# Kernel tuning notes

Measured on AMD Instinct MI355X. Metric: run time of the kernel, lower is better.

## Reference

```python
import jax, jax.numpy as jnp
import numpy as np

B, S, E, NUM_CLASSES = 4, 4096, 256, 16

def setup_inputs() -> dict:
    key = jax.random.key(0)
    ks = jax.random.split(key, 10)
    std = E ** -0.5
    return {
        "x":  jax.random.normal(ks[0], (B, S, E), dtype=jnp.float32),
        "wq": jax.random.normal(ks[1], (E, E), dtype=jnp.float32) * std,
        "bq": jnp.zeros((E,), dtype=jnp.float32),
        "wk": jax.random.normal(ks[2], (E, E), dtype=jnp.float32) * std,
        "bk": jnp.zeros((E,), dtype=jnp.float32),
        "wv": jax.random.normal(ks[3], (E, E), dtype=jnp.float32) * std,
        "bv": jnp.zeros((E,), dtype=jnp.float32),
        "wo": jax.random.normal(ks[4], (NUM_CLASSES, E), dtype=jnp.float32) * std,
        "bo": jnp.zeros((NUM_CLASSES,), dtype=jnp.float32),
    }

def reference(x, wq, bq, wk, bk, wv, bv, wo, bo):
    embed_dim = wq.shape[0]
    scaling = embed_dim ** -0.5  # float(embed_dim) ** (-0.5)
    # torch Linear: y = x @ W.T + b
    Q = jnp.einsum('bse,oe->bso', x, wq) + bq
    K = jnp.einsum('bse,oe->bso', x, wk) + bk
    V = jnp.einsum('bse,oe->bso', x, wv) + bv
    # scores: [B, S, S]
    scores = jnp.einsum('bqe,bke->bqk', Q, K) * scaling
    # original code has `/ (embed_dim ^ 0.5)`; intended math is / sqrt(embed_dim)
    attn = jax.nn.softmax(scores, axis=-1) * scaling
    attn_out = jnp.einsum('bqk,bke->bqe', attn, V)
    return jnp.einsum('bqe,oe->bqo', attn_out, wo) + bo
```

## Files before the change

### kernel.cpp

```cpp
#include <hip/hip_runtime.h>
#include <hip/hip_bf16.h>


#define S_ 4096
#define E_ 256
#define B_ 4
#define NC_ 16
#define BS_ (B_ * S_)
#define NS_ 4

typedef __attribute__((ext_vector_type(8))) short bf16x8;
typedef __attribute__((ext_vector_type(4))) float f32x4;

__device__ __forceinline__ unsigned short bf16_rtne(float f) {
    unsigned int u = __float_as_uint(f);
    return (unsigned short)((u + 0x7FFFu + ((u >> 16) & 1u)) >> 16);
}
__device__ __forceinline__ bf16x8 pack8(f32x4 a, f32x4 b) {
    bf16x8 r;
#pragma unroll
    for (int i = 0; i < 4; i++) r[i] = (short)bf16_rtne(a[i]);
#pragma unroll
    for (int i = 0; i < 4; i++) r[4 + i] = (short)bf16_rtne(b[i]);
    return r;
}
__device__ __forceinline__ void gl_lds16(const void* g, void* lds) {
    __builtin_amdgcn_global_load_lds(
        (const __attribute__((address_space(1))) unsigned int*)g,
        (__attribute__((address_space(3))) unsigned int*)lds, 16, 0, 0);
}
__device__ __forceinline__ int swz_u(int q) { return q ^ ((q >> 3) & 7); }

#define XUNITS_ (BS_ * E_ / 8)
#define WUNITS_ (3 * E_ * E_ / 8)
__global__ __launch_bounds__(256) void pack_xw(
    const float* __restrict__ x, const float* __restrict__ wq,
    const float* __restrict__ wk, const float* __restrict__ wv,
    short* __restrict__ xb, short* __restrict__ wb) {
    int u = blockIdx.x * 256 + threadIdx.x;
    const float* src;
    short* dst;
    if (u < XUNITS_) {
        src = x + (size_t)u * 8;
        dst = xb + (size_t)u * 8;
    } else {
        int u2 = u - XUNITS_;
        int sel = u2 >> 13;
        int off = (u2 & 8191) * 8;
        src = ((sel == 0) ? wq : (sel == 1) ? wk : wv) + off;
        dst = wb + sel * (E_ * E_) + off;
    }
    f32x4 a = *(const f32x4*)src;
    f32x4 b = *(const f32x4*)(src + 4);
    *(bf16x8*)dst = pack8(a, b);
}

__global__ __launch_bounds__(256) void qkv_gemm(
    const short* __restrict__ xb, const short* __restrict__ wb,
    const float* __restrict__ bq, const float* __restrict__ bk,
    const float* __restrict__ bv, short* __restrict__ Qb,
    short* __restrict__ Kb, short* __restrict__ Vtc) {
    __shared__ __align__(16) short stg[2][10240];
    __shared__ __align__(16) short epi[16896];

    int t = threadIdx.x;
    int lin = blockIdx.x;
    int xcd = lin & 7, r8 = lin >> 3;
    int sel = r8 >> 5;
    int m0 = (((xcd << 5) | (r8 & 31))) * 64;
    int lane = t & 63, wid = t >> 6, quad = lane >> 4, idx = lane & 15;

    const short* wsel = wb + sel * (E_ * E_);
    const float* bias = (sel == 0) ? bq : (sel == 1) ? bk : bv;

    int ux = swz_u(t);
    const short* xsrc = xb + (size_t)(m0 + (ux >> 2)) * E_ + (ux & 3) * 8;
    const short* wsrc[4];
#pragma unroll
    for (int i = 0; i < 4; i++) {
        int q = i * 256 + t, u = swz_u(q);
        wsrc[i] = wsel + (size_t)(u >> 2) * E_ + (u & 3) * 8;
    }

    gl_lds16(xsrc, &stg[0][t * 8]);
#pragma unroll
    for (int i = 0; i < 4; i++) gl_lds16(wsrc[i], &stg[0][(256 + i * 256 + t) * 8]);

    f32x4 zf = {0.f, 0.f, 0.f, 0.f};
    f32x4 acc[16];
#pragma unroll
    for (int i = 0; i < 16; i++) acc[i] = zf;

    int fo = (idx * 4 + quad) ^ (idx >> 1);

    for (int it = 0; it < 8; it++) {
        __syncthreads();
        if (it < 7) {
            int kc = (it + 1) * 32;
            short* d = stg[(it + 1) & 1];
            gl_lds16(xsrc + kc, &d[t * 8]);
#pragma unroll
            for (int i = 0; i < 4; i++)
                gl_lds16(wsrc[i] + kc, &d[(256 + i * 256 + t) * 8]);
        }
        const short* cb = stg[it & 1];
        bf16x8 af = *(const bf16x8*)&cb[(wid * 64 + fo) * 8];
        const short* cw = &cb[(256 + fo) * 8];
        __builtin_amdgcn_s_setprio(1);
#pragma unroll
        for (int ct = 0; ct < 16; ct++)
            acc[ct] = __builtin_amdgcn_mfma_f32_16x16x32_bf16(
                af, *(const bf16x8*)&cw[ct * 512], acc[ct], 0, 0, 0);
        __builtin_amdgcn_s_setprio(0);
    }

    int qr = quad * 4;
    if (sel == 2) {
#pragma unroll
        for (int ct = 0; ct < 16; ct++) {
            int e = ct * 16 + idx;
            float bb = bias[e];
#pragma unroll
            for (int r = 0; r < 4; r++) {
                int mr = wid * 16 + qr + r;
                int ckg = mr >> 5, sin = mr & 31;
                int sp = ((sin & 15) << 1) | (sin >> 4);
                int pos = (sp >> 3) ^ ((e >> 1) & 3);
                epi[ckg * 8192 + e * 32 + pos * 8 + (sp & 7)] =
                    (short)bf16_rtne(acc[ct][r] + bb);
            }
        }
        __syncthreads();
        size_t base = ((size_t)((m0 >> 12) * 128 + ((m0 & (S_ - 1)) >> 5))) * 8192;
#pragma unroll
        for (int j = 0; j < 8; j++) {
            int unit = j * 256 + t;
            *(bf16x8*)(Vtc + base + (size_t)unit * 8) = *(const bf16x8*)&epi[unit * 8];
        }
    } else {
        float alpha = (sel == 0) ? 0.0625f : 1.0f;
#pragma unroll
        for (int ct = 0; ct < 16; ct++) {
            int n = ct * 16 + idx;
            float bb = bias[n];
#pragma unroll
            for (int r = 0; r < 4; r++) {
                int row = wid * 16 + qr + r;
                int col = (sel == 1) ? ((((n >> 3) ^ (row & 7)) << 3) | (n & 7)) : n;
                epi[row * 264 + col] = (short)bf16_rtne((acc[ct][r] + bb) * alpha);
            }
        }
        __syncthreads();
        short* out = (sel == 0) ? Qb : Kb;
#pragma unroll
        for (int j = 0; j < 8; j++) {
            int g = j * 256 + t;
            int row = g >> 5, seg = g & 31;
            *(bf16x8*)(out + (size_t)(m0 + row) * E_ + seg * 8) =
                *(const bf16x8*)&epi[row * 264 + seg * 8];
        }
    }
}

__global__ __launch_bounds__(256, 2) void flash_attn(
    const short* __restrict__ Qb, const short* __restrict__ Kb,
    const short* __restrict__ Vtc, short* __restrict__ Opart,
    float* __restrict__ lpart) {
    __shared__ __align__(16) short lds[37888];

    int t = threadIdx.x;
    int lin = blockIdx.x;
    int xcd = lin & 7, r8 = lin >> 3;
    int pair = (xcd << 1) | (r8 >> 5);
    int b = pair >> 2, slice = pair & 3, q0 = (r8 & 31) * 128;
    int key0 = slice * (S_ / NS_);
    const int nchunk = (S_ / NS_) / 32;
    int lane = t & 63, wv = t >> 6, quad = lane >> 4, idx = lane & 15;

    bf16x8 qf[2][8];
#pragma unroll
    for (int u = 0; u < 2; u++) {
        const short* qrow = Qb + (size_t)(b * S_ + q0 + u * 64 + wv * 16 + idx) * E_ + quad * 8;
#pragma unroll
        for (int c = 0; c < 8; c++) qf[u][c] = *(const bf16x8*)(qrow + c * 32);
    }

    f32x4 zf = {0.f, 0.f, 0.f, 0.f};
    f32x4 oacc[2][16];
#pragma unroll
    for (int u = 0; u < 2; u++)
#pragma unroll
        for (int i = 0; i < 16; i++) oacc[u][i] = zf;
    float ls[2][4] = {{0, 0, 0, 0}, {0, 0, 0, 0}};

    const short* kg = Kb + (size_t)(b * S_ + key0) * E_ + lane * 8;
    const short* vg = Vtc + ((size_t)(b * 128 + (key0 >> 5))) * 8192 + lane * 8;
    short* psw = lds + 32768 + wv * 1280;
    unsigned int* pswu = (unsigned int*)psw;
    int vsw = (quad ^ ((idx >> 1) & 3)) << 3;

#pragma unroll
    for (int j = 0; j < 4; j++) gl_lds16(kg + (wv * 4 + j) * 512, &lds[(wv * 4 + j) * 512]);
#pragma unroll
    for (int j = 0; j < 4; j++) gl_lds16(vg + (wv * 4 + j) * 512, &lds[16384 + (wv * 4 + j) * 512]);
#pragma unroll
    for (int j = 0; j < 4; j++) gl_lds16(kg + 8192 + (wv * 4 + j) * 512, &lds[8192 + (wv * 4 + j) * 512]);
    __syncthreads();

    {
        f32x4 s[4] = {zf, zf, zf, zf};
        __builtin_amdgcn_s_setprio(1);
#pragma unroll
        for (int c = 0; c < 8; c++) {
            int p = (((c * 4 + quad) ^ (idx & 7)) << 3);
            bf16x8 k0 = *(const bf16x8*)&lds[idx * 256 + p];
            bf16x8 k1 = *(const bf16x8*)&lds[(16 + idx) * 256 + p];
            s[0] = __builtin_amdgcn_mfma_f32_16x16x32_bf16(qf[0][c], k0, s[0], 0, 0, 0);
            s[1] = __builtin_amdgcn_mfma_f32_16x16x32_bf16(qf[0][c], k1, s[1], 0, 0, 0);
            s[2] = __builtin_amdgcn_mfma_f32_16x16x32_bf16(qf[1][c], k0, s[2], 0, 0, 0);
            s[3] = __builtin_amdgcn_mfma_f32_16x16x32_bf16(qf[1][c], k1, s[3], 0, 0, 0);
        }
        __builtin_amdgcn_s_setprio(0);
#pragma unroll
        for (int u = 0; u < 2; u++)
#pragma unroll
            for (int r = 0; r < 4; r++) {
                float p0 = __expf(s[u * 2][r]);
                float p1 = __expf(s[u * 2 + 1][r]);
                ls[u][r] += p0 + p1;
                pswu[u * 320 + (quad * 4 + r) * 20 + idx] =
                    (unsigned int)bf16_rtne(p0) | ((unsigned int)bf16_rtne(p1) << 16);
            }
    }

    for (int ck = 0; ck < nchunk - 1; ck++) {
        __syncthreads();
        if (ck + 2 < nchunk) {
            const short* ks = kg + (size_t)(ck + 2) * 8192;
            short* kd = lds + (ck & 1) * 8192;
#pragma unroll
            for (int j = 0; j < 4; j++) gl_lds16(ks + (wv * 4 + j) * 512, &kd[(wv * 4 + j) * 512]);
        }
        {
            const short* vs = vg + (size_t)(ck + 1) * 8192;
            short* vd = lds + 16384 + ((ck + 1) & 1) * 8192;
#pragma unroll
            for (int j = 0; j < 4; j++) gl_lds16(vs + (wv * 4 + j) * 512, &vd[(wv * 4 + j) * 512]);
        }
        const short* kc = lds + ((ck + 1) & 1) * 8192;
        f32x4 s[4] = {zf, zf, zf, zf};
        __builtin_amdgcn_s_setprio(1);
#pragma unroll
        for (int c = 0; c < 8; c++) {
            int p = (((c * 4 + quad) ^ (idx & 7)) << 3);
            bf16x8 k0 = *(const bf16x8*)&kc[idx * 256 + p];
            bf16x8 k1 = *(const bf16x8*)&kc[(16 + idx) * 256 + p];
            s[0] = __builtin_amdgcn_mfma_f32_16x16x32_bf16(qf[0][c], k0, s[0], 0, 0, 0);
            s[1] = __builtin_amdgcn_mfma_f32_16x16x32_bf16(qf[0][c], k1, s[1], 0, 0, 0);
            s[2] = __builtin_amdgcn_mfma_f32_16x16x32_bf16(qf[1][c], k0, s[2], 0, 0, 0);
            s[3] = __builtin_amdgcn_mfma_f32_16x16x32_bf16(qf[1][c], k1, s[3], 0, 0, 0);
        }
        __builtin_amdgcn_s_setprio(0);
        bf16x8 af0 = *(const bf16x8*)&psw[idx * 40 + quad * 8];
        bf16x8 af1 = *(const bf16x8*)&psw[640 + idx * 40 + quad * 8];
#pragma unroll
        for (int u = 0; u < 2; u++)
#pragma unroll
            for (int r = 0; r < 4; r++) {
                float p0 = __expf(s[u * 2][r]);
                float p1 = __expf(s[u * 2 + 1][r]);
                ls[u][r] += p0 + p1;
                pswu[u * 320 + (quad * 4 + r) * 20 + idx] =
                    (unsigned int)bf16_rtne(p0) | ((unsigned int)bf16_rtne(p1) << 16);
            }
        const short* vc = lds + 16384 + (ck & 1) * 8192;
        __builtin_amdgcn_s_setprio(1);
#pragma unroll
        for (int ct = 0; ct < 16; ct++) {
            bf16x8 v = *(const bf16x8*)&vc[(ct * 16 + idx) * 32 + vsw];
            oacc[0][ct] = __builtin_amdgcn_mfma_f32_16x16x32_bf16(af0, v, oacc[0][ct], 0, 0, 0);
            oacc[1][ct] = __builtin_amdgcn_mfma_f32_16x16x32_bf16(af1, v, oacc[1][ct], 0, 0, 0);
        }
        __builtin_amdgcn_s_setprio(0);
    }
    __syncthreads();
    {
        bf16x8 af0 = *(const bf16x8*)&psw[idx * 40 + quad * 8];
        bf16x8 af1 = *(const bf16x8*)&psw[640 + idx * 40 + quad * 8];
        const short* vc = lds + 16384 + ((nchunk - 1) & 1) * 8192;
        __builtin_amdgcn_s_setprio(1);
#pragma unroll
        for (int ct = 0; ct < 16; ct++) {
            bf16x8 v = *(const bf16x8*)&vc[(ct * 16 + idx) * 32 + vsw];
            oacc[0][ct] = __builtin_amdgcn_mfma_f32_16x16x32_bf16(af0, v, oacc[0][ct], 0, 0, 0);
            oacc[1][ct] = __builtin_amdgcn_mfma_f32_16x16x32_bf16(af1, v, oacc[1][ct], 0, 0, 0);
        }
        __builtin_amdgcn_s_setprio(0);
    }
    __syncthreads();

#pragma unroll
    for (int u = 0; u < 2; u++)
#pragma unroll
        for (int r = 0; r < 4; r++) {
            float v = ls[u][r];
            v += __shfl_xor(v, 1);
            v += __shfl_xor(v, 2);
            v += __shfl_xor(v, 4);
            v += __shfl_xor(v, 8);
            if (idx == 0)
                lpart[(size_t)slice * BS_ + b * S_ + q0 + u * 64 + wv * 16 + quad * 4 + r] = v;
        }

    short* scr = lds + wv * 8192;
#pragma unroll
    for (int u = 0; u < 2; u++)
#pragma unroll
        for (int ct = 0; ct < 16; ct++) {
            int e = ct * 16 + idx;
#pragma unroll
            for (int r = 0; r < 4; r++) {
                int lr = quad * 4 + r;
                scr[u * 4096 + lr * 256 + ((((e >> 3) ^ (lr & 7)) << 3) | (e & 7))] =
                    (short)bf16_rtne(oacc[u][ct][r]);
            }
        }
#pragma unroll
    for (int u = 0; u < 2; u++) {
        size_t obase = ((size_t)slice * BS_ + (size_t)b * S_ + q0 + u * 64 + wv * 16) * E_;
#pragma unroll
        for (int j = 0; j < 8; j++) {
            int unit = j * 64 + lane;
            *(bf16x8*)(Opart + obase + (size_t)unit * 8) =
                *(const bf16x8*)&scr[u * 4096 + unit * 8];
        }
    }
}

__global__ __launch_bounds__(256) void proj_out(
    const short* __restrict__ Opart, const float* __restrict__ lpart,
    const float* __restrict__ wo, const float* __restrict__ bo,
    float* __restrict__ out) {
    __shared__ __align__(16) short at2[2][16384];
    int t = threadIdx.x;
    int m0 = blockIdx.x * 64;
    int lane = t & 63, wv = t >> 6, quad = lane >> 4, idx = lane & 15;

    bf16x8 bw[8];
#pragma unroll
    for (int c = 0; c < 8; c++) {
        const float* ws = wo + idx * E_ + c * 32 + quad * 8;
        f32x4 w0 = *(const f32x4*)ws;
        f32x4 w1 = *(const f32x4*)(ws + 4);
        bw[c] = pack8(w0, w1);
    }

#pragma unroll
    for (int j = 0; j < 8; j++)
        gl_lds16(Opart + (size_t)m0 * E_ + (wv * 8 + j) * 512 + lane * 8,
                 &at2[0][(wv * 8 + j) * 512]);

    f32x4 acc = {0.f, 0.f, 0.f, 0.f};
    for (int ns = 0; ns < NS_; ns++) {
        __syncthreads();
        if (ns + 1 < NS_) {
            const short* src = Opart + ((size_t)(ns + 1) * BS_ + m0) * E_ + lane * 8;
#pragma unroll
            for (int j = 0; j < 8; j++)
                gl_lds16(src + (wv * 8 + j) * 512, &at2[(ns + 1) & 1][(wv * 8 + j) * 512]);
        }
        const short* a = at2[ns & 1];
#pragma unroll
        for (int c = 0; c < 8; c++) {
            bf16x8 af = *(const bf16x8*)&a[(wv * 16 + idx) * 256 +
                                           ((((c * 4 + quad) ^ (idx & 7)) << 3))];
            acc = __builtin_amdgcn_mfma_f32_16x16x32_bf16(af, bw[c], acc, 0, 0, 0);
        }
    }
#pragma unroll
    for (int r = 0; r < 4; r++) {
        int m = m0 + wv * 16 + quad * 4 + r;
        float ltot = 0.f;
#pragma unroll
        for (int ns = 0; ns < NS_; ns++) ltot += lpart[(size_t)ns * BS_ + m];
        out[(size_t)m * NC_ + idx] = acc[r] * (0.0625f / ltot) + bo[idx];
    }
}

extern "C" void kernel_launch(void* const* d_in, const int* in_sizes, int n_in,
                              void* d_out, int out_size, void* d_ws, size_t ws_size,
                              hipStream_t stream) {
    const float* x  = (const float*)d_in[0];
    const float* wq = (const float*)d_in[1];
    const float* bq = (const float*)d_in[2];
    const float* wk = (const float*)d_in[3];
    const float* bk = (const float*)d_in[4];
    const float* wv = (const float*)d_in[5];
    const float* bv = (const float*)d_in[6];
    const float* wo = (const float*)d_in[7];
    const float* bo = (const float*)d_in[8];
    float* out = (float*)d_out;

    const size_t NEL = (size_t)BS_ * E_;
    short* Qb = (short*)d_ws;
    short* Kb = Qb + NEL;
    short* Vtc = Kb + NEL;
    short* Opart = Vtc + NEL;
    float* lpart = (float*)(Opart + (size_t)NS_ * NEL);
    short* xb = Opart;
    short* wb = Opart + NEL;

    pack_xw<<<(XUNITS_ + WUNITS_) / 256, 256, 0, stream>>>(x, wq, wk, wv, xb, wb);
    qkv_gemm<<<dim3(768), 256, 0, stream>>>(xb, wb, bq, bk, bv, Qb, Kb, Vtc);
    flash_attn<<<dim3(512), 256, 0, stream>>>(Qb, Kb, Vtc, Opart, lpart);
    proj_out<<<BS_ / 64, 256, 0, stream>>>(Opart, lpart, wo, bo, out);
}
```

Before: 176.7 us.

## Fuse output projection into flash attention epilogue with atomic partial sums

The flash attention kernel now multiplies its per-slice unnormalized output tile by the bf16-packed output weights and atomically adds the 16-class partials into a zeroed fp32 buffer. This removes writing and re-reading the four bf16 partial attention outputs (BS×E per slice). A small norm_out kernel then applies the softmax denominator, scaling and bias. The pack kernel also packs wo and zeroes the partial buffer. The P-fragment LDS loads are hoisted to the top of the loop. Atomics add contention and make the summation order nondeterministic.

```diff
diff --git a/kernel.cpp b/kernel.cpp
--- a/kernel.cpp
+++ b/kernel.cpp
@@ -33,22 +33,36 @@
 
 #define XUNITS_ (BS_ * E_ / 8)
 #define WUNITS_ (3 * E_ * E_ / 8)
+#define WOUNITS_ (NC_ * E_ / 8)
+#define ZUNITS_ (BS_ * NC_ / 8)
 __global__ __launch_bounds__(256) void pack_xw(
     const float* __restrict__ x, const float* __restrict__ wq,
     const float* __restrict__ wk, const float* __restrict__ wv,
-    short* __restrict__ xb, short* __restrict__ wb) {
+    const float* __restrict__ wo, short* __restrict__ xb,
+    short* __restrict__ wb, short* __restrict__ wbo,
+    float* __restrict__ partial) {
     int u = blockIdx.x * 256 + threadIdx.x;
     const float* src;
     short* dst;
     if (u < XUNITS_) {
         src = x + (size_t)u * 8;
         dst = xb + (size_t)u * 8;
-    } else {
+    } else if (u < XUNITS_ + WUNITS_) {
         int u2 = u - XUNITS_;
         int sel = u2 >> 13;
         int off = (u2 & 8191) * 8;
         src = ((sel == 0) ? wq : (sel == 1) ? wk : wv) + off;
         dst = wb + sel * (E_ * E_) + off;
+    } else if (u < XUNITS_ + WUNITS_ + WOUNITS_) {
+        int u2 = u - (XUNITS_ + WUNITS_);
+        src = wo + (size_t)u2 * 8;
+        dst = wbo + (size_t)u2 * 8;
+    } else {
+        int zu = u - (XUNITS_ + WUNITS_ + WOUNITS_);
+        f32x4 z = {0.f, 0.f, 0.f, 0.f};
+        ((f32x4*)partial)[zu * 2] = z;
+        ((f32x4*)partial)[zu * 2 + 1] = z;
+        return;
     }
     f32x4 a = *(const f32x4*)src;
     f32x4 b = *(const f32x4*)(src + 4);
@@ -164,8 +178,8 @@
 
 __global__ __launch_bounds__(256, 2) void flash_attn(
     const short* __restrict__ Qb, const short* __restrict__ Kb,
-    const short* __restrict__ Vtc, short* __restrict__ Opart,
-    float* __restrict__ lpart) {
+    const short* __restrict__ Vtc, const short* __restrict__ wbo,
+    float* __restrict__ partial, float* __restrict__ lpart) {
     __shared__ __align__(16) short lds[37888];
 
     int t = threadIdx.x;
@@ -235,6 +249,8 @@
 
     for (int ck = 0; ck < nchunk - 1; ck++) {
         __syncthreads();
+        bf16x8 af0 = *(const bf16x8*)&psw[idx * 40 + quad * 8];
+        bf16x8 af1 = *(const bf16x8*)&psw[640 + idx * 40 + quad * 8];
         if (ck + 2 < nchunk) {
             const short* ks = kg + (size_t)(ck + 2) * 8192;
             short* kd = lds + (ck & 1) * 8192;
@@ -261,8 +277,6 @@
             s[3] = __builtin_amdgcn_mfma_f32_16x16x32_bf16(qf[1][c], k1, s[3], 0, 0, 0);
         }
         __builtin_amdgcn_s_setprio(0);
-        bf16x8 af0 = *(const bf16x8*)&psw[idx * 40 + quad * 8];
-        bf16x8 af1 = *(const bf16x8*)&psw[640 + idx * 40 + quad * 8];
 #pragma unroll
         for (int u = 0; u < 2; u++)
 #pragma unroll
@@ -325,66 +339,37 @@
                     (short)bf16_rtne(oacc[u][ct][r]);
             }
         }
-#pragma unroll
-    for (int u = 0; u < 2; u++) {
-        size_t obase = ((size_t)slice * BS_ + (size_t)b * S_ + q0 + u * 64 + wv * 16) * E_;
-#pragma unroll
-        for (int j = 0; j < 8; j++) {
-            int unit = j * 64 + lane;
-            *(bf16x8*)(Opart + obase + (size_t)unit * 8) =
-                *(const bf16x8*)&scr[u * 4096 + unit * 8];
-        }
-    }
-}
-
-__global__ __launch_bounds__(256) void proj_out(
-    const short* __restrict__ Opart, const float* __restrict__ lpart,
-    const float* __restrict__ wo, const float* __restrict__ bo,
-    float* __restrict__ out) {
-    __shared__ __align__(16) short at2[2][16384];
+
+    f32x4 pacc[2] = {zf, zf};
+#pragma unroll
+    for (int c = 0; c < 8; c++) {
+        bf16x8 bw = *(const bf16x8*)(wbo + idx * E_ + c * 32 + quad * 8);
+#pragma unroll
+        for (int u = 0; u < 2; u++) {
+            bf16x8 af = *(const bf16x8*)&scr[u * 4096 + idx * 256 +
+                                             (((c * 4 + quad) ^ (idx & 7)) << 3)];
+            pacc[u] = __builtin_amdgcn_mfma_f32_16x16x32_bf16(af, bw, pacc[u], 0, 0, 0);
+        }
+    }
+#pragma unroll
+    for (int u = 0; u < 2; u++)
+#pragma unroll
+        for (int r = 0; r < 4; r++) {
+            int m = q0 + u * 64 + wv * 16 + quad * 4 + r;
+            atomicAdd(&partial[((size_t)b * S_ + m) * NC_ + idx], pacc[u][r]);
+        }
+}
+
+__global__ __launch_bounds__(256) void norm_out(
+    const float* __restrict__ partial, const float* __restrict__ lpart,
+    const float* __restrict__ bo, float* __restrict__ out) {
     int t = threadIdx.x;
-    int m0 = blockIdx.x * 64;
-    int lane = t & 63, wv = t >> 6, quad = lane >> 4, idx = lane & 15;
-
-    bf16x8 bw[8];
-#pragma unroll
-    for (int c = 0; c < 8; c++) {
-        const float* ws = wo + idx * E_ + c * 32 + quad * 8;
-        f32x4 w0 = *(const f32x4*)ws;
-        f32x4 w1 = *(const f32x4*)(ws + 4);
-        bw[c] = pack8(w0, w1);
-    }
-
-#pragma unroll
-    for (int j = 0; j < 8; j++)
-        gl_lds16(Opart + (size_t)m0 * E_ + (wv * 8 + j) * 512 + lane * 8,
-                 &at2[0][(wv * 8 + j) * 512]);
-
-    f32x4 acc = {0.f, 0.f, 0.f, 0.f};
-    for (int ns = 0; ns < NS_; ns++) {
-        __syncthreads();
-        if (ns + 1 < NS_) {
-            const short* src = Opart + ((size_t)(ns + 1) * BS_ + m0) * E_ + lane * 8;
-#pragma unroll
-            for (int j = 0; j < 8; j++)
-                gl_lds16(src + (wv * 8 + j) * 512, &at2[(ns + 1) & 1][(wv * 8 + j) * 512]);
-        }
-        const short* a = at2[ns & 1];
-#pragma unroll
-        for (int c = 0; c < 8; c++) {
-            bf16x8 af = *(const bf16x8*)&a[(wv * 16 + idx) * 256 +
-                                           ((((c * 4 + quad) ^ (idx & 7)) << 3))];
-            acc = __builtin_amdgcn_mfma_f32_16x16x32_bf16(af, bw[c], acc, 0, 0, 0);
-        }
-    }
-#pragma unroll
-    for (int r = 0; r < 4; r++) {
-        int m = m0 + wv * 16 + quad * 4 + r;
-        float ltot = 0.f;
-#pragma unroll
-        for (int ns = 0; ns < NS_; ns++) ltot += lpart[(size_t)ns * BS_ + m];
-        out[(size_t)m * NC_ + idx] = acc[r] * (0.0625f / ltot) + bo[idx];
-    }
+    int m = blockIdx.x * 16 + (t >> 4), o = t & 15;
+    float ltot = 0.f;
+#pragma unroll
+    for (int ns = 0; ns < NS_; ns++) ltot += lpart[(size_t)ns * BS_ + m];
+    size_t i = (size_t)m * NC_ + o;
+    out[i] = partial[i] * (0.0625f / ltot) + bo[o];
 }
 
 extern "C" void kernel_launch(void* const* d_in, const int* in_sizes, int n_in,
@@ -405,13 +390,15 @@
     short* Qb = (short*)d_ws;
     short* Kb = Qb + NEL;
     short* Vtc = Kb + NEL;
-    short* Opart = Vtc + NEL;
-    float* lpart = (float*)(Opart + (size_t)NS_ * NEL);
-    short* xb = Opart;
-    short* wb = Opart + NEL;
-
-    pack_xw<<<(XUNITS_ + WUNITS_) / 256, 256, 0, stream>>>(x, wq, wk, wv, xb, wb);
+    short* xb = Vtc + NEL;
+    short* wb = xb + NEL;
+    short* wbo = wb + (size_t)3 * E_ * E_;
+    float* partial = (float*)(wbo + (size_t)NC_ * E_);
+    float* lpart = partial + (size_t)BS_ * NC_;
+
+    pack_xw<<<(XUNITS_ + WUNITS_ + WOUNITS_ + ZUNITS_) / 256, 256, 0, stream>>>(
+        x, wq, wk, wv, wo, xb, wb, wbo, partial);
     qkv_gemm<<<dim3(768), 256, 0, stream>>>(xb, wb, bq, bk, bv, Qb, Kb, Vtc);
-    flash_attn<<<dim3(512), 256, 0, stream>>>(Qb, Kb, Vtc, Opart, lpart);
-    proj_out<<<BS_ / 64, 256, 0, stream>>>(Opart, lpart, wo, bo, out);
-}
+    flash_attn<<<dim3(512), 256, 0, stream>>>(Qb, Kb, Vtc, wbo, partial, lpart);
+    norm_out<<<dim3(BS_ / 16), 256, 0, stream>>>(partial, lpart, bo, out);
+}
```

New measurement: 170.3 us. -3.6%, faster.
